# Performance work log

Measured on AMD Instinct MI355X. Metric: run time of the kernel, lower is better.

Reference implementation:

```python
import jax, jax.numpy as jnp
import numpy as np

EPS = 1e-06
FOCUSING_FACTOR = 3


def setup_inputs() -> dict:
    key = jax.random.key(0)
    k1, k2, k3, k4, k5 = jax.random.split(key, 5)
    N, L, H, D = 8, 4096, 8, 64
    return {
        "queries": jax.random.normal(k1, (N, L, H, D), dtype=jnp.float32),
        "keys": jax.random.normal(k2, (N, L, H, D), dtype=jnp.float32),
        "values": jax.random.normal(k3, (N, L, H, D), dtype=jnp.float32),
        "scale_param": jnp.zeros((1, 1, 1, D), dtype=jnp.float32),
        "dwc_w": jax.random.normal(k4, (D, 1, 5, 5), dtype=jnp.float32) * 0.1,
        "dwc_b": jax.random.normal(k5, (D,), dtype=jnp.float32) * 0.1,
        "height": 64,
    }


def reference(queries, keys, values, scale_param, dwc_w, dwc_b, height):
    N, L, H, D = values.shape
    width = L // height

    scale = jax.nn.softplus(scale_param)  # [1,1,1,D]
    q = (jax.nn.relu(queries) + 1e-06) / scale
    k = (jax.nn.relu(keys) + 1e-06) / scale

    q_norm = jnp.linalg.norm(q, axis=-1, keepdims=True)
    k_norm = jnp.linalg.norm(k, axis=-1, keepdims=True)
    q = q ** FOCUSING_FACTOR
    k = k ** FOCUSING_FACTOR
    q = q / jnp.linalg.norm(q, axis=-1, keepdims=True) * q_norm
    k = k / jnp.linalg.norm(k, axis=-1, keepdims=True) * k_norm

    # linear attention: kv summary [N,H,D,D], normalizer z [N,L,H]
    kv = jnp.einsum("nshd,nshv->nhdv", k, values)
    z = 1.0 / (jnp.einsum("nlhd,nhd->nlh", q, k.sum(axis=1)) + EPS)
    o = jnp.einsum("nlhd,nhdv,nlh->nlhv", q, kv, z)

    # depthwise 5x5 conv on values: 'n (h w) heads d -> (n heads) d h w'
    vf = values.reshape(N, height, width, H, D)
    vf = vf.transpose(0, 3, 4, 1, 2).reshape(N * H, D, height, width)
    vf = jax.lax.conv_general_dilated(
        vf, dwc_w,
        window_strides=(1, 1), padding=((2, 2), (2, 2)),
        dimension_numbers=("NCHW", "OIHW", "NCHW"),
        feature_group_count=D,
    ) + dwc_b[None, :, None, None]
    vf = vf.reshape(N, H, D, height, width).transpose(0, 3, 4, 1, 2)
    vf = vf.reshape(N, L, H, D)

    return o + vf
```

## Files before the change

### kernel.cpp

```cpp
#include <hip/hip_runtime.h>

typedef __attribute__((ext_vector_type(8))) short short8;
typedef __attribute__((ext_vector_type(4))) float f32x4;

#define LSEQ   4096
#define NHEAD  8
#define DCH    64
#define HEIGHT 64
#define WIDTH  64

static __device__ __forceinline__ float bfu2f(unsigned short u) {
  return __uint_as_float(((unsigned int)u) << 16);
}
static __device__ __forceinline__ unsigned short f2bfu(float f) {
  unsigned int b = __float_as_uint(f);
  b += 0x7FFFu + ((b >> 16) & 1u);
  return (unsigned short)(b >> 16);
}
static __device__ __forceinline__ float ldf(const void* p, int i, int isbf) {
  return isbf ? bfu2f(((const unsigned short*)p)[i]) : ((const float*)p)[i];
}
static __device__ __forceinline__ float softplus_inv(float sp) {
  float s = (sp > 20.f) ? sp : log1pf(expf(sp));
  return 1.f / s;
}
static __device__ __forceinline__ void unpack2(unsigned int u, float& lo, float& hi) {
  lo = __uint_as_float(u << 16);
  hi = __uint_as_float(u & 0xFFFF0000u);
}
static __device__ __forceinline__ void load8(const void* p, int gi, int isbf, float o[8]) {
  if (isbf) {
    uint4 u = *(const uint4*)((const unsigned short*)p + gi);
    unpack2(u.x, o[0], o[1]); unpack2(u.y, o[2], o[3]);
    unpack2(u.z, o[4], o[5]); unpack2(u.w, o[6], o[7]);
  } else {
    const float4* f4 = (const float4*)((const float*)p + gi);
    float4 a = f4[0], b = f4[1];
    o[0]=a.x; o[1]=a.y; o[2]=a.z; o[3]=a.w;
    o[4]=b.x; o[5]=b.y; o[6]=b.z; o[7]=b.w;
  }
}
static __device__ __forceinline__ void row_reduce2(float& a, float& b) {
  #pragma unroll
  for (int m = 1; m < 8; m <<= 1) { a += __shfl_xor(a, m, 64); b += __shfl_xor(b, m, 64); }
}
static __device__ __forceinline__ float row_reduce1(float a) {
  #pragma unroll
  for (int m = 1; m < 8; m <<= 1) a += __shfl_xor(a, m, 64);
  return a;
}

__global__ void detect_kernel(const unsigned int* __restrict__ q, int* __restrict__ flag) {
  int lane = threadIdx.x & 63;
  int hits = 0;
  #pragma unroll
  for (int i = 0; i < 4; ++i) {
    unsigned int lo = q[lane * 4 + i] & 0xFFFFu;
    unsigned int e  = (lo >> 7) & 0xFFu;
    if (lo == 0u || (e >= 110u && e <= 140u)) hits++;
  }
  #pragma unroll
  for (int m = 1; m < 64; m <<= 1) hits += __shfl_xor(hits, m, 64);
  if (lane == 0) *flag = (hits > 128) ? 1 : 0;
}

__global__ __launch_bounds__(256) void kv_kernel(
    const void* __restrict__ keys, const void* __restrict__ values,
    const void* __restrict__ scale_param,
    float* __restrict__ kv_p, float* __restrict__ ksum_g,
    const int* __restrict__ flagp, int chunks, int rows)
{
  __shared__ __align__(16) unsigned short kfT[64 * 40];
  __shared__ __align__(16) unsigned short vvT[64 * 40];
  __shared__ float red[256];

  const int isbf = *flagp;
  const int b = blockIdx.x;
  const int chunk = b % chunks;
  const int nh = b / chunks;
  const int h = nh & 7, n = nh >> 3;
  const int t = threadIdx.x, lane = t & 63, wid = t >> 6;
  const int quad = lane >> 4, m16 = lane & 15;
  const int r = lane >> 3, c = lane & 7, d0 = c * 8;
  const int s_local = wid * 8 + r;
  const int sp = s_local ^ ((c & 3) << 3);

  float inv_s[8];
  #pragma unroll
  for (int i = 0; i < 8; ++i) inv_s[i] = softplus_inv(ldf(scale_param, d0 + i, isbf));

  f32x4 acc[4];
  #pragma unroll
  for (int mt = 0; mt < 4; ++mt) acc[mt] = (f32x4){0.f, 0.f, 0.f, 0.f};
  float ksum_acc[8];
  #pragma unroll
  for (int i = 0; i < 8; ++i) ksum_acc[i] = 0.f;

  const int nsub = rows >> 5;
  for (int sub = 0; sub < nsub; ++sub) {
    const int s = chunk * rows + sub * 32 + s_local;
    const int gi = ((n * LSEQ + s) * NHEAD + h) * DCH + d0;

    float kraw[8];
    load8(keys, gi, isbf, kraw);
    float xv[8], yv[8], s2 = 0.f, s6 = 0.f;
    #pragma unroll
    for (int i = 0; i < 8; ++i) {
      xv[i] = (fmaxf(kraw[i], 0.f) + 1e-6f) * inv_s[i];
      s2 += xv[i] * xv[i];
    }
    #pragma unroll
    for (int i = 0; i < 8; ++i) {
      yv[i] = xv[i] * xv[i] * xv[i];
      s6 += yv[i] * yv[i];
    }
    row_reduce2(s2, s6);
    const float coef = sqrtf(s2 / s6);
    #pragma unroll
    for (int i = 0; i < 8; ++i) {
      float f = yv[i] * coef;
      ksum_acc[i] += f;
      kfT[(d0 + i) * 40 + sp] = f2bfu(f);
    }
    if (isbf) {
      uint4 u = *(const uint4*)((const unsigned short*)values + gi);
      unsigned short vs[8];
      *(uint4*)vs = u;
      #pragma unroll
      for (int i = 0; i < 8; ++i) vvT[(d0 + i) * 40 + sp] = vs[i];
    } else {
      float vraw[8];
      load8(values, gi, 0, vraw);
      #pragma unroll
      for (int i = 0; i < 8; ++i) vvT[(d0 + i) * 40 + sp] = f2bfu(vraw[i]);
    }
    __syncthreads();

    const int v = wid * 16 + m16;
    short8 bfr = *(const short8*)&vvT[v * 40 + (quad ^ ((v >> 3) & 3)) * 8];
    #pragma unroll
    for (int mt = 0; mt < 4; ++mt) {
      int d = mt * 16 + m16;
      short8 afr = *(const short8*)&kfT[d * 40 + (quad ^ ((d >> 3) & 3)) * 8];
      acc[mt] = __builtin_amdgcn_mfma_f32_16x16x32_bf16(afr, bfr, acc[mt], 0, 0, 0);
    }
    __syncthreads();
  }

  float* dst = kv_p + ((size_t)chunk * 64 + nh) * 4096;
  #pragma unroll
  for (int mt = 0; mt < 4; ++mt)
    #pragma unroll
    for (int rr = 0; rr < 4; ++rr) {
      int d = mt * 16 + quad * 4 + rr;
      dst[d * 64 + wid * 16 + m16] = acc[mt][rr];
    }

  #pragma unroll
  for (int i = 0; i < 8; ++i) {
    #pragma unroll
    for (int m = 8; m < 64; m <<= 1) ksum_acc[i] += __shfl_xor(ksum_acc[i], m, 64);
  }
  if (r == 0) {
    #pragma unroll
    for (int i = 0; i < 8; ++i) red[wid * 64 + d0 + i] = ksum_acc[i];
  }
  __syncthreads();
  if (t < 64) {
    float tot = red[t] + red[64 + t] + red[128 + t] + red[192 + t];
    atomicAdd(&ksum_g[nh * 64 + t], tot);
  }
}

__global__ __launch_bounds__(256) void reduce_kernel(
    const float* __restrict__ kv_p, unsigned short* __restrict__ kvb, int chunks)
{
  int cidx = blockIdx.x * 256 + threadIdx.x;
  int nh = cidx >> 12;
  int dv = cidx & 4095;
  int d = dv >> 6, v = dv & 63;
  float s = 0.f;
  for (int ch = 0; ch < chunks; ++ch)
    s += kv_p[((size_t)ch * 64 + nh) * 4096 + dv];
  kvb[(nh * 64 + v) * 64 + d] = f2bfu(s);
}

__global__ __launch_bounds__(256) void attn_kernel(
    const void* __restrict__ queries, const unsigned short* __restrict__ kvb,
    const float* __restrict__ ksum_g, const void* __restrict__ scale_param,
    void* __restrict__ out, const int* __restrict__ flagp)
{
  __shared__ __align__(16) unsigned short qf[64 * 72];

  const int isbf = *flagp;
  const int b = blockIdx.x;
  const int y = b & 63;
  const int nh = b >> 6;
  const int h = nh & 7, n = nh >> 3;
  const int t = threadIdx.x, lane = t & 63, wid = t >> 6;
  const int quad = lane >> 4, m16 = lane & 15;
  const int r = lane >> 3, c = lane & 7, d0 = c * 8;

  float inv_s[8];
  #pragma unroll
  for (int i = 0; i < 8; ++i) inv_s[i] = softplus_inv(ldf(scale_param, d0 + i, isbf));
  float ks[8];
  {
    float4 k0 = *(const float4*)&ksum_g[nh * 64 + d0];
    float4 k1 = *(const float4*)&ksum_g[nh * 64 + d0 + 4];
    ks[0]=k0.x; ks[1]=k0.y; ks[2]=k0.z; ks[3]=k0.w;
    ks[4]=k1.x; ks[5]=k1.y; ks[6]=k1.z; ks[7]=k1.w;
  }

  const unsigned short* kvrow = kvb + (nh * 64 + wid * 16 + m16) * 64;
  short8 bfr0 = *(const short8*)&kvrow[quad * 8];
  short8 bfr1 = *(const short8*)&kvrow[32 + quad * 8];

  #pragma unroll
  for (int batch = 0; batch < 2; ++batch) {
    int x = wid * 16 + batch * 8 + r;
    int gi = ((n * LSEQ + y * 64 + x) * NHEAD + h) * DCH + d0;
    float qraw[8];
    load8(queries, gi, isbf, qraw);
    float xv[8], yv[8], s2 = 0.f, s6 = 0.f;
    #pragma unroll
    for (int i = 0; i < 8; ++i) {
      xv[i] = (fmaxf(qraw[i], 0.f) + 1e-6f) * inv_s[i];
      s2 += xv[i] * xv[i];
    }
    #pragma unroll
    for (int i = 0; i < 8; ++i) {
      yv[i] = xv[i] * xv[i] * xv[i];
      s6 += yv[i] * yv[i];
    }
    row_reduce2(s2, s6);
    const float coef = sqrtf(s2 / s6);
    float f[8], dot = 0.f;
    #pragma unroll
    for (int i = 0; i < 8; ++i) { f[i] = yv[i] * coef; dot += f[i] * ks[i]; }
    dot = row_reduce1(dot);
    const float z = 1.f / (dot + 1e-6f);
    uint4 pk;
    pk.x = (unsigned int)f2bfu(f[0] * z) | ((unsigned int)f2bfu(f[1] * z) << 16);
    pk.y = (unsigned int)f2bfu(f[2] * z) | ((unsigned int)f2bfu(f[3] * z) << 16);
    pk.z = (unsigned int)f2bfu(f[4] * z) | ((unsigned int)f2bfu(f[5] * z) << 16);
    pk.w = (unsigned int)f2bfu(f[6] * z) | ((unsigned int)f2bfu(f[7] * z) << 16);
    *(uint4*)&qf[x * 72 + d0] = pk;
  }
  __syncthreads();

  const size_t obase = (((size_t)n * LSEQ + y * 64) * NHEAD + h) * DCH;
  #pragma unroll
  for (int mt = 0; mt < 4; ++mt) {
    f32x4 acc = (f32x4){0.f, 0.f, 0.f, 0.f};
    short8 a0 = *(const short8*)&qf[(mt * 16 + m16) * 72 + quad * 8];
    short8 a1 = *(const short8*)&qf[(mt * 16 + m16) * 72 + 32 + quad * 8];
    acc = __builtin_amdgcn_mfma_f32_16x16x32_bf16(a0, bfr0, acc, 0, 0, 0);
    acc = __builtin_amdgcn_mfma_f32_16x16x32_bf16(a1, bfr1, acc, 0, 0, 0);
    #pragma unroll
    for (int rr = 0; rr < 4; ++rr) {
      int x = mt * 16 + quad * 4 + rr;
      int v = wid * 16 + m16;
      size_t oi = obase + (size_t)x * (NHEAD * DCH) + v;
      if (isbf) ((unsigned short*)out)[oi] = f2bfu(acc[rr]);
      else      ((float*)out)[oi] = acc[rr];
    }
  }
}

__global__ __launch_bounds__(256) void conv_kernel(
    const void* __restrict__ values, const void* __restrict__ dwc_w,
    const void* __restrict__ dwc_b, void* __restrict__ out,
    const int* __restrict__ flagp)
{
  __shared__ __align__(16) unsigned short vs[8 * 64 * 64];
  __shared__ float wl[25 * 64];
  __shared__ float bl[64];

  const int isbf = *flagp;
  const int b = blockIdx.x;
  const int slab = b & 15;
  const int nh = b >> 4;
  const int h = nh & 7, n = nh >> 3;
  const int y0 = slab * 4;
  const int t = threadIdx.x;

  for (int i = t; i < 25 * 64; i += 256) {
    int d = i / 25, tap = i - d * 25;
    wl[tap * 64 + d] = ldf(dwc_w, i, isbf);
  }
  if (t < 64) bl[t] = ldf(dwc_b, t, isbf);

  for (int it = t; it < 8 * 64 * 8; it += 256) {
    int j = it & 7;
    int xx = (it >> 3) & 63;
    int rr = it >> 9;
    int yy = y0 - 2 + rr;
    unsigned short* dst = &vs[((rr * 64 + xx) * 64) + ((j ^ (xx & 7)) * 8)];
    if (yy >= 0 && yy < HEIGHT) {
      int gi = ((n * LSEQ + yy * 64 + xx) * NHEAD + h) * DCH + j * 8;
      if (isbf) {
        *(uint4*)dst = *(const uint4*)((const unsigned short*)values + gi);
      } else {
        const float4* s4 = (const float4*)((const float*)values + gi);
        float4 f0 = s4[0], f1 = s4[1];
        dst[0] = f2bfu(f0.x); dst[1] = f2bfu(f0.y);
        dst[2] = f2bfu(f0.z); dst[3] = f2bfu(f0.w);
        dst[4] = f2bfu(f1.x); dst[5] = f2bfu(f1.y);
        dst[6] = f2bfu(f1.z); dst[7] = f2bfu(f1.w);
      }
    } else {
      uint4 z; z.x = z.y = z.z = z.w = 0u;
      *(uint4*)dst = z;
    }
  }
  __syncthreads();

  const int xx = t & 63, jb = t >> 6;
  for (int jj = jb; jj < 8; jj += 4) {
    float a[4][8];
    float bias8[8];
    {
      float4 b0 = *(const float4*)&bl[jj * 8];
      float4 b1 = *(const float4*)&bl[jj * 8 + 4];
      bias8[0]=b0.x; bias8[1]=b0.y; bias8[2]=b0.z; bias8[3]=b0.w;
      bias8[4]=b1.x; bias8[5]=b1.y; bias8[6]=b1.z; bias8[7]=b1.w;
    }
    #pragma unroll
    for (int rr = 0; rr < 4; ++rr)
      #pragma unroll
      for (int cc = 0; cc < 8; ++cc) a[rr][cc] = bias8[cc];

    for (int ky = 0; ky < 5; ++ky) {
      #pragma unroll
      for (int kx = 0; kx < 5; ++kx) {
        int xs = xx + kx - 2;
        if ((unsigned)xs < (unsigned)WIDTH) {
          float4 w0 = *(const float4*)&wl[(ky * 5 + kx) * 64 + jj * 8];
          float4 w1 = *(const float4*)&wl[(ky * 5 + kx) * 64 + jj * 8 + 4];
          #pragma unroll
          for (int rr = 0; rr < 4; ++rr) {
            uint4 pv = *(const uint4*)&vs[(((rr + ky) * 64 + xs) * 64) + ((jj ^ (xs & 7)) * 8)];
            float v0,v1,v2,v3,v4,v5,v6,v7;
            unpack2(pv.x, v0, v1); unpack2(pv.y, v2, v3);
            unpack2(pv.z, v4, v5); unpack2(pv.w, v6, v7);
            a[rr][0] += w0.x * v0; a[rr][1] += w0.y * v1;
            a[rr][2] += w0.z * v2; a[rr][3] += w0.w * v3;
            a[rr][4] += w1.x * v4; a[rr][5] += w1.y * v5;
            a[rr][6] += w1.z * v6; a[rr][7] += w1.w * v7;
          }
        }
      }
    }
    #pragma unroll
    for (int rr = 0; rr < 4; ++rr) {
      size_t oi = (((size_t)n * LSEQ + (y0 + rr) * 64 + xx) * NHEAD + h) * DCH + jj * 8;
      if (isbf) {
        unsigned short* op = (unsigned short*)out + oi;
        uint4 cur = *(uint4*)op;
        float c0,c1,c2,c3,c4,c5,c6,c7;
        unpack2(cur.x, c0, c1); unpack2(cur.y, c2, c3);
        unpack2(cur.z, c4, c5); unpack2(cur.w, c6, c7);
        uint4 res;
        res.x = (unsigned int)f2bfu(c0 + a[rr][0]) | ((unsigned int)f2bfu(c1 + a[rr][1]) << 16);
        res.y = (unsigned int)f2bfu(c2 + a[rr][2]) | ((unsigned int)f2bfu(c3 + a[rr][3]) << 16);
        res.z = (unsigned int)f2bfu(c4 + a[rr][4]) | ((unsigned int)f2bfu(c5 + a[rr][5]) << 16);
        res.w = (unsigned int)f2bfu(c6 + a[rr][6]) | ((unsigned int)f2bfu(c7 + a[rr][7]) << 16);
        *(uint4*)op = res;
      } else {
        float* op = (float*)out + oi;
        float4 o0 = *(float4*)op;
        float4 o1 = *(float4*)(op + 4);
        o0.x += a[rr][0]; o0.y += a[rr][1]; o0.z += a[rr][2]; o0.w += a[rr][3];
        o1.x += a[rr][4]; o1.y += a[rr][5]; o1.z += a[rr][6]; o1.w += a[rr][7];
        *(float4*)op = o0;
        *(float4*)(op + 4) = o1;
      }
    }
  }
}

extern "C" void kernel_launch(void* const* d_in, const int* in_sizes, int n_in,
                              void* d_out, int out_size, void* d_ws, size_t ws_size,
                              hipStream_t stream) {
  int chunks = 16;
  while (chunks > 1) {
    size_t need = (size_t)chunks * 64 * 4096 * 4 + 64 * 4096 * 2 + 4096 * 4 + 64;
    if (need <= ws_size) break;
    chunks >>= 1;
  }
  const int rows = LSEQ / chunks;

  float* kv_p = (float*)d_ws;
  unsigned short* kvb = (unsigned short*)(kv_p + (size_t)chunks * 64 * 4096);
  float* ksum = (float*)(kvb + 64 * 4096);
  int* flag = (int*)(ksum + 4096);

  hipMemsetAsync(ksum, 0, 4096 * sizeof(float), stream);
  detect_kernel<<<1, 64, 0, stream>>>((const unsigned int*)d_in[0], flag);
  kv_kernel<<<64 * chunks, 256, 0, stream>>>(
      d_in[1], d_in[2], d_in[3], kv_p, ksum, flag, chunks, rows);
  reduce_kernel<<<1024, 256, 0, stream>>>(kv_p, kvb, chunks);
  attn_kernel<<<4096, 256, 0, stream>>>(
      d_in[0], kvb, ksum, d_in[3], d_out, flag);
  conv_kernel<<<64 * 16, 256, 0, stream>>>(
      d_in[2], d_in[4], d_in[5], d_out, flag);
}
```

Baseline: 334.1 us.

## Fuse attention output and depthwise conv into one kernel; double kv tile depth

Merges attn_kernel and conv_kernel into a single kernel that computes the linear-attention output for a 4-row slab, keeps it in LDS as bf16, then adds the depthwise 5x5 conv, which reads values directly from global memory instead of staging them in LDS. This removes the write and read-modify-write of the output in global memory. The kv_kernel now processes 64 rows per sync step instead of 32, issuing two MFMAs per step. Block ids are remapped so slabs are grouped by xcd. The attention result is rounded to bf16 before the conv term is added, which costs some precision in the fp32 path.

```diff
diff --git a/kernel.cpp b/kernel.cpp
--- a/kernel.cpp
+++ b/kernel.cpp
@@ -70,8 +70,8 @@
     float* __restrict__ kv_p, float* __restrict__ ksum_g,
     const int* __restrict__ flagp, int chunks, int rows)
 {
-  __shared__ __align__(16) unsigned short kfT[64 * 40];
-  __shared__ __align__(16) unsigned short vvT[64 * 40];
+  __shared__ __align__(16) unsigned short kfT[64 * 72];
+  __shared__ __align__(16) unsigned short vvT[64 * 72];
   __shared__ float red[256];
 
   const int isbf = *flagp;
@@ -82,8 +82,7 @@
   const int t = threadIdx.x, lane = t & 63, wid = t >> 6;
   const int quad = lane >> 4, m16 = lane & 15;
   const int r = lane >> 3, c = lane & 7, d0 = c * 8;
-  const int s_local = wid * 8 + r;
-  const int sp = s_local ^ ((c & 3) << 3);
+  const int swz = (c & 3) << 3;
 
   float inv_s[8];
   #pragma unroll
@@ -96,53 +95,63 @@
   #pragma unroll
   for (int i = 0; i < 8; ++i) ksum_acc[i] = 0.f;
 
-  const int nsub = rows >> 5;
+  const int nsub = rows >> 6;
   for (int sub = 0; sub < nsub; ++sub) {
-    const int s = chunk * rows + sub * 32 + s_local;
-    const int gi = ((n * LSEQ + s) * NHEAD + h) * DCH + d0;
-
-    float kraw[8];
-    load8(keys, gi, isbf, kraw);
-    float xv[8], yv[8], s2 = 0.f, s6 = 0.f;
-    #pragma unroll
-    for (int i = 0; i < 8; ++i) {
-      xv[i] = (fmaxf(kraw[i], 0.f) + 1e-6f) * inv_s[i];
-      s2 += xv[i] * xv[i];
-    }
-    #pragma unroll
-    for (int i = 0; i < 8; ++i) {
-      yv[i] = xv[i] * xv[i] * xv[i];
-      s6 += yv[i] * yv[i];
-    }
-    row_reduce2(s2, s6);
-    const float coef = sqrtf(s2 / s6);
-    #pragma unroll
-    for (int i = 0; i < 8; ++i) {
-      float f = yv[i] * coef;
-      ksum_acc[i] += f;
-      kfT[(d0 + i) * 40 + sp] = f2bfu(f);
-    }
-    if (isbf) {
-      uint4 u = *(const uint4*)((const unsigned short*)values + gi);
-      unsigned short vs[8];
-      *(uint4*)vs = u;
-      #pragma unroll
-      for (int i = 0; i < 8; ++i) vvT[(d0 + i) * 40 + sp] = vs[i];
-    } else {
-      float vraw[8];
-      load8(values, gi, 0, vraw);
-      #pragma unroll
-      for (int i = 0; i < 8; ++i) vvT[(d0 + i) * 40 + sp] = f2bfu(vraw[i]);
+    #pragma unroll
+    for (int pp = 0; pp < 2; ++pp) {
+      const int s_loc = wid * 8 + r + pp * 32;
+      const int sp = s_loc ^ swz;
+      const int s = chunk * rows + sub * 64 + s_loc;
+      const int gi = ((n * LSEQ + s) * NHEAD + h) * DCH + d0;
+
+      float kraw[8];
+      load8(keys, gi, isbf, kraw);
+      float xv[8], yv[8], s2 = 0.f, s6 = 0.f;
+      #pragma unroll
+      for (int i = 0; i < 8; ++i) {
+        xv[i] = (fmaxf(kraw[i], 0.f) + 1e-6f) * inv_s[i];
+        s2 += xv[i] * xv[i];
+      }
+      #pragma unroll
+      for (int i = 0; i < 8; ++i) {
+        yv[i] = xv[i] * xv[i] * xv[i];
+        s6 += yv[i] * yv[i];
+      }
+      row_reduce2(s2, s6);
+      const float coef = sqrtf(s2 / s6);
+      #pragma unroll
+      for (int i = 0; i < 8; ++i) {
+        float f = yv[i] * coef;
+        ksum_acc[i] += f;
+        kfT[(d0 + i) * 72 + sp] = f2bfu(f);
+      }
+      if (isbf) {
+        uint4 u = *(const uint4*)((const unsigned short*)values + gi);
+        unsigned short vs[8];
+        *(uint4*)vs = u;
+        #pragma unroll
+        for (int i = 0; i < 8; ++i) vvT[(d0 + i) * 72 + sp] = vs[i];
+      } else {
+        float vraw[8];
+        load8(values, gi, 0, vraw);
+        #pragma unroll
+        for (int i = 0; i < 8; ++i) vvT[(d0 + i) * 72 + sp] = f2bfu(vraw[i]);
+      }
     }
     __syncthreads();
 
     const int v = wid * 16 + m16;
-    short8 bfr = *(const short8*)&vvT[v * 40 + (quad ^ ((v >> 3) & 3)) * 8];
+    const int vg = (v >> 3) & 3;
+    short8 bv0 = *(const short8*)&vvT[v * 72 + ((quad ^ vg) << 3)];
+    short8 bv1 = *(const short8*)&vvT[v * 72 + ((4 + (quad ^ vg)) << 3)];
     #pragma unroll
     for (int mt = 0; mt < 4; ++mt) {
       int d = mt * 16 + m16;
-      short8 afr = *(const short8*)&kfT[d * 40 + (quad ^ ((d >> 3) & 3)) * 8];
-      acc[mt] = __builtin_amdgcn_mfma_f32_16x16x32_bf16(afr, bfr, acc[mt], 0, 0, 0);
+      int dg = (d >> 3) & 3;
+      short8 a0 = *(const short8*)&kfT[d * 72 + ((quad ^ dg) << 3)];
+      short8 a1 = *(const short8*)&kfT[d * 72 + ((4 + (quad ^ dg)) << 3)];
+      acc[mt] = __builtin_amdgcn_mfma_f32_16x16x32_bf16(a0, bv0, acc[mt], 0, 0, 0);
+      acc[mt] = __builtin_amdgcn_mfma_f32_16x16x32_bf16(a1, bv1, acc[mt], 0, 0, 0);
     }
     __syncthreads();
   }
@@ -185,21 +194,33 @@
   kvb[(nh * 64 + v) * 64 + d] = f2bfu(s);
 }
 
-__global__ __launch_bounds__(256) void attn_kernel(
-    const void* __restrict__ queries, const unsigned short* __restrict__ kvb,
-    const float* __restrict__ ksum_g, const void* __restrict__ scale_param,
-    void* __restrict__ out, const int* __restrict__ flagp)
+__global__ __launch_bounds__(256) void fused_kernel(
+    const void* __restrict__ queries, const void* __restrict__ values,
+    const unsigned short* __restrict__ kvb, const float* __restrict__ ksum_g,
+    const void* __restrict__ scale_param, const void* __restrict__ dwc_w,
+    const void* __restrict__ dwc_b, void* __restrict__ out,
+    const int* __restrict__ flagp)
 {
-  __shared__ __align__(16) unsigned short qf[64 * 72];
+  __shared__ __align__(16) unsigned short qfo[256 * 72];
+  __shared__ float wl[25 * 64];
+  __shared__ float bl[64];
 
   const int isbf = *flagp;
   const int b = blockIdx.x;
-  const int y = b & 63;
-  const int nh = b >> 6;
+  const int xcd = b & 7;
+  const int rest = b >> 3;
+  const int nh = rest & 63;
+  const int y0 = xcd * 8 + (rest >> 6) * 4;
   const int h = nh & 7, n = nh >> 3;
   const int t = threadIdx.x, lane = t & 63, wid = t >> 6;
   const int quad = lane >> 4, m16 = lane & 15;
   const int r = lane >> 3, c = lane & 7, d0 = c * 8;
+
+  for (int i = t; i < 25 * 64; i += 256) {
+    int d = i / 25, tap = i - d * 25;
+    wl[tap * 64 + d] = ldf(dwc_w, i, isbf);
+  }
+  if (t < 64) bl[t] = ldf(dwc_b, t, isbf);
 
   float inv_s[8];
   #pragma unroll
@@ -212,14 +233,11 @@
     ks[4]=k1.x; ks[5]=k1.y; ks[6]=k1.z; ks[7]=k1.w;
   }
 
-  const unsigned short* kvrow = kvb + (nh * 64 + wid * 16 + m16) * 64;
-  short8 bfr0 = *(const short8*)&kvrow[quad * 8];
-  short8 bfr1 = *(const short8*)&kvrow[32 + quad * 8];
-
-  #pragma unroll
-  for (int batch = 0; batch < 2; ++batch) {
-    int x = wid * 16 + batch * 8 + r;
-    int gi = ((n * LSEQ + y * 64 + x) * NHEAD + h) * DCH + d0;
+  #pragma unroll
+  for (int batch = 0; batch < 8; ++batch) {
+    int p = wid * 64 + batch * 8 + r;
+    int x = p & 63, yy = y0 + (p >> 6);
+    int gi = ((n * LSEQ + yy * 64 + x) * NHEAD + h) * DCH + d0;
     float qraw[8];
     load8(queries, gi, isbf, qraw);
     float xv[8], yv[8], s2 = 0.f, s6 = 0.f;
@@ -245,136 +263,119 @@
     pk.y = (unsigned int)f2bfu(f[2] * z) | ((unsigned int)f2bfu(f[3] * z) << 16);
     pk.z = (unsigned int)f2bfu(f[4] * z) | ((unsigned int)f2bfu(f[5] * z) << 16);
     pk.w = (unsigned int)f2bfu(f[6] * z) | ((unsigned int)f2bfu(f[7] * z) << 16);
-    *(uint4*)&qf[x * 72 + d0] = pk;
+    *(uint4*)&qfo[p * 72 + d0] = pk;
   }
   __syncthreads();
 
-  const size_t obase = (((size_t)n * LSEQ + y * 64) * NHEAD + h) * DCH;
-  #pragma unroll
-  for (int mt = 0; mt < 4; ++mt) {
-    f32x4 acc = (f32x4){0.f, 0.f, 0.f, 0.f};
-    short8 a0 = *(const short8*)&qf[(mt * 16 + m16) * 72 + quad * 8];
-    short8 a1 = *(const short8*)&qf[(mt * 16 + m16) * 72 + 32 + quad * 8];
-    acc = __builtin_amdgcn_mfma_f32_16x16x32_bf16(a0, bfr0, acc, 0, 0, 0);
-    acc = __builtin_amdgcn_mfma_f32_16x16x32_bf16(a1, bfr1, acc, 0, 0, 0);
-    #pragma unroll
-    for (int rr = 0; rr < 4; ++rr) {
-      int x = mt * 16 + quad * 4 + rr;
-      int v = wid * 16 + m16;
-      size_t oi = obase + (size_t)x * (NHEAD * DCH) + v;
-      if (isbf) ((unsigned short*)out)[oi] = f2bfu(acc[rr]);
-      else      ((float*)out)[oi] = acc[rr];
-    }
-  }
-}
-
-__global__ __launch_bounds__(256) void conv_kernel(
-    const void* __restrict__ values, const void* __restrict__ dwc_w,
-    const void* __restrict__ dwc_b, void* __restrict__ out,
-    const int* __restrict__ flagp)
-{
-  __shared__ __align__(16) unsigned short vs[8 * 64 * 64];
-  __shared__ float wl[25 * 64];
-  __shared__ float bl[64];
-
-  const int isbf = *flagp;
-  const int b = blockIdx.x;
-  const int slab = b & 15;
-  const int nh = b >> 4;
-  const int h = nh & 7, n = nh >> 3;
-  const int y0 = slab * 4;
-  const int t = threadIdx.x;
-
-  for (int i = t; i < 25 * 64; i += 256) {
-    int d = i / 25, tap = i - d * 25;
-    wl[tap * 64 + d] = ldf(dwc_w, i, isbf);
-  }
-  if (t < 64) bl[t] = ldf(dwc_b, t, isbf);
-
-  for (int it = t; it < 8 * 64 * 8; it += 256) {
-    int j = it & 7;
-    int xx = (it >> 3) & 63;
-    int rr = it >> 9;
-    int yy = y0 - 2 + rr;
-    unsigned short* dst = &vs[((rr * 64 + xx) * 64) + ((j ^ (xx & 7)) * 8)];
-    if (yy >= 0 && yy < HEIGHT) {
-      int gi = ((n * LSEQ + yy * 64 + xx) * NHEAD + h) * DCH + j * 8;
-      if (isbf) {
-        *(uint4*)dst = *(const uint4*)((const unsigned short*)values + gi);
-      } else {
-        const float4* s4 = (const float4*)((const float*)values + gi);
-        float4 f0 = s4[0], f1 = s4[1];
-        dst[0] = f2bfu(f0.x); dst[1] = f2bfu(f0.y);
-        dst[2] = f2bfu(f0.z); dst[3] = f2bfu(f0.w);
-        dst[4] = f2bfu(f1.x); dst[5] = f2bfu(f1.y);
-        dst[6] = f2bfu(f1.z); dst[7] = f2bfu(f1.w);
-      }
-    } else {
-      uint4 z; z.x = z.y = z.z = z.w = 0u;
-      *(uint4*)dst = z;
-    }
+  const int v = wid * 16 + m16;
+  const unsigned short* kvrow = kvb + (nh * 64 + v) * 64;
+  short8 bfr0 = *(const short8*)&kvrow[quad * 8];
+  short8 bfr1 = *(const short8*)&kvrow[32 + quad * 8];
+  f32x4 acc[16];
+  #pragma unroll
+  for (int mt = 0; mt < 16; ++mt) {
+    acc[mt] = (f32x4){0.f, 0.f, 0.f, 0.f};
+    short8 a0 = *(const short8*)&qfo[(mt * 16 + m16) * 72 + quad * 8];
+    short8 a1 = *(const short8*)&qfo[(mt * 16 + m16) * 72 + 32 + quad * 8];
+    acc[mt] = __builtin_amdgcn_mfma_f32_16x16x32_bf16(a0, bfr0, acc[mt], 0, 0, 0);
+    acc[mt] = __builtin_amdgcn_mfma_f32_16x16x32_bf16(a1, bfr1, acc[mt], 0, 0, 0);
   }
   __syncthreads();
 
+  #pragma unroll
+  for (int mt = 0; mt < 16; ++mt)
+    #pragma unroll
+    for (int rg = 0; rg < 4; ++rg) {
+      int p = mt * 16 + quad * 4 + rg;
+      qfo[p * 72 + v] = f2bfu(acc[mt][rg]);
+    }
+
   const int xx = t & 63, jb = t >> 6;
-  for (int jj = jb; jj < 8; jj += 4) {
-    float a[4][8];
-    float bias8[8];
+  float ca[2][4][8];
+  #pragma unroll
+  for (int ji = 0; ji < 2; ++ji) {
+    const int jj = jb + ji * 4;
     {
       float4 b0 = *(const float4*)&bl[jj * 8];
       float4 b1 = *(const float4*)&bl[jj * 8 + 4];
-      bias8[0]=b0.x; bias8[1]=b0.y; bias8[2]=b0.z; bias8[3]=b0.w;
-      bias8[4]=b1.x; bias8[5]=b1.y; bias8[6]=b1.z; bias8[7]=b1.w;
-    }
-    #pragma unroll
-    for (int rr = 0; rr < 4; ++rr)
-      #pragma unroll
-      for (int cc = 0; cc < 8; ++cc) a[rr][cc] = bias8[cc];
-
-    for (int ky = 0; ky < 5; ++ky) {
+      #pragma unroll
+      for (int rr = 0; rr < 4; ++rr) {
+        ca[ji][rr][0]=b0.x; ca[ji][rr][1]=b0.y; ca[ji][rr][2]=b0.z; ca[ji][rr][3]=b0.w;
+        ca[ji][rr][4]=b1.x; ca[ji][rr][5]=b1.y; ca[ji][rr][6]=b1.z; ca[ji][rr][7]=b1.w;
+      }
+    }
+    #pragma unroll
+    for (int z = 0; z < 8; ++z) {
+      int yy = y0 - 2 + z;
+      if (yy < 0 || yy >= HEIGHT) continue;
+      float win[5][8];
       #pragma unroll
       for (int kx = 0; kx < 5; ++kx) {
         int xs = xx + kx - 2;
-        if ((unsigned)xs < (unsigned)WIDTH) {
+        bool ok = (unsigned)xs < (unsigned)WIDTH;
+        if (isbf) {
+          uint4 pv = {0u,0u,0u,0u};
+          if (ok) pv = *(const uint4*)((const unsigned short*)values +
+                       (((n * LSEQ + yy * 64 + xs) * NHEAD + h) * DCH + jj * 8));
+          unpack2(pv.x, win[kx][0], win[kx][1]); unpack2(pv.y, win[kx][2], win[kx][3]);
+          unpack2(pv.z, win[kx][4], win[kx][5]); unpack2(pv.w, win[kx][6], win[kx][7]);
+        } else {
+          float4 a = {0,0,0,0}, bq = {0,0,0,0};
+          if (ok) {
+            const float4* f4 = (const float4*)((const float*)values +
+                       (((n * LSEQ + yy * 64 + xs) * NHEAD + h) * DCH + jj * 8));
+            a = f4[0]; bq = f4[1];
+          }
+          win[kx][0]=a.x; win[kx][1]=a.y; win[kx][2]=a.z; win[kx][3]=a.w;
+          win[kx][4]=bq.x; win[kx][5]=bq.y; win[kx][6]=bq.z; win[kx][7]=bq.w;
+        }
+      }
+      #pragma unroll
+      for (int ky = 0; ky < 5; ++ky) {
+        const int rr = z - ky;
+        if (rr < 0 || rr > 3) continue;
+        #pragma unroll
+        for (int kx = 0; kx < 5; ++kx) {
           float4 w0 = *(const float4*)&wl[(ky * 5 + kx) * 64 + jj * 8];
           float4 w1 = *(const float4*)&wl[(ky * 5 + kx) * 64 + jj * 8 + 4];
-          #pragma unroll
-          for (int rr = 0; rr < 4; ++rr) {
-            uint4 pv = *(const uint4*)&vs[(((rr + ky) * 64 + xs) * 64) + ((jj ^ (xs & 7)) * 8)];
-            float v0,v1,v2,v3,v4,v5,v6,v7;
-            unpack2(pv.x, v0, v1); unpack2(pv.y, v2, v3);
-            unpack2(pv.z, v4, v5); unpack2(pv.w, v6, v7);
-            a[rr][0] += w0.x * v0; a[rr][1] += w0.y * v1;
-            a[rr][2] += w0.z * v2; a[rr][3] += w0.w * v3;
-            a[rr][4] += w1.x * v4; a[rr][5] += w1.y * v5;
-            a[rr][6] += w1.z * v6; a[rr][7] += w1.w * v7;
-          }
+          ca[ji][rr][0] += w0.x * win[kx][0]; ca[ji][rr][1] += w0.y * win[kx][1];
+          ca[ji][rr][2] += w0.z * win[kx][2]; ca[ji][rr][3] += w0.w * win[kx][3];
+          ca[ji][rr][4] += w1.x * win[kx][4]; ca[ji][rr][5] += w1.y * win[kx][5];
+          ca[ji][rr][6] += w1.z * win[kx][6]; ca[ji][rr][7] += w1.w * win[kx][7];
         }
       }
     }
+  }
+  __syncthreads();
+
+  #pragma unroll
+  for (int ji = 0; ji < 2; ++ji) {
+    const int jj = jb + ji * 4;
     #pragma unroll
     for (int rr = 0; rr < 4; ++rr) {
+      int p = rr * 64 + xx;
+      uint4 ov = *(const uint4*)&qfo[p * 72 + jj * 8];
+      float o0,o1,o2,o3,o4,o5,o6,o7;
+      unpack2(ov.x, o0, o1); unpack2(ov.y, o2, o3);
+      unpack2(ov.z, o4, o5); unpack2(ov.w, o6, o7);
+      float r0 = o0 + ca[ji][rr][0], r1 = o1 + ca[ji][rr][1];
+      float r2 = o2 + ca[ji][rr][2], r3 = o3 + ca[ji][rr][3];
+      float r4 = o4 + ca[ji][rr][4], r5 = o5 + ca[ji][rr][5];
+      float r6 = o6 + ca[ji][rr][6], r7 = o7 + ca[ji][rr][7];
       size_t oi = (((size_t)n * LSEQ + (y0 + rr) * 64 + xx) * NHEAD + h) * DCH + jj * 8;
       if (isbf) {
-        unsigned short* op = (unsigned short*)out + oi;
-        uint4 cur = *(uint4*)op;
-        float c0,c1,c2,c3,c4,c5,c6,c7;
-        unpack2(cur.x, c0, c1); unpack2(cur.y, c2, c3);
-        unpack2(cur.z, c4, c5); unpack2(cur.w, c6, c7);
         uint4 res;
-        res.x = (unsigned int)f2bfu(c0 + a[rr][0]) | ((unsigned int)f2bfu(c1 + a[rr][1]) << 16);
-        res.y = (unsigned int)f2bfu(c2 + a[rr][2]) | ((unsigned int)f2bfu(c3 + a[rr][3]) << 16);
-        res.z = (unsigned int)f2bfu(c4 + a[rr][4]) | ((unsigned int)f2bfu(c5 + a[rr][5]) << 16);
-        res.w = (unsigned int)f2bfu(c6 + a[rr][6]) | ((unsigned int)f2bfu(c7 + a[rr][7]) << 16);
-        *(uint4*)op = res;
+        res.x = (unsigned int)f2bfu(r0) | ((unsigned int)f2bfu(r1) << 16);
+        res.y = (unsigned int)f2bfu(r2) | ((unsigned int)f2bfu(r3) << 16);
+        res.z = (unsigned int)f2bfu(r4) | ((unsigned int)f2bfu(r5) << 16);
+        res.w = (unsigned int)f2bfu(r6) | ((unsigned int)f2bfu(r7) << 16);
+        *(uint4*)((unsigned short*)out + oi) = res;
       } else {
         float* op = (float*)out + oi;
-        float4 o0 = *(float4*)op;
-        float4 o1 = *(float4*)(op + 4);
-        o0.x += a[rr][0]; o0.y += a[rr][1]; o0.z += a[rr][2]; o0.w += a[rr][3];
-        o1.x += a[rr][4]; o1.y += a[rr][5]; o1.z += a[rr][6]; o1.w += a[rr][7];
-        *(float4*)op = o0;
-        *(float4*)(op + 4) = o1;
+        float4 q0 = {r0, r1, r2, r3};
+        float4 q1 = {r4, r5, r6, r7};
+        *(float4*)op = q0;
+        *(float4*)(op + 4) = q1;
       }
     }
   }
@@ -401,8 +402,6 @@
   kv_kernel<<<64 * chunks, 256, 0, stream>>>(
       d_in[1], d_in[2], d_in[3], kv_p, ksum, flag, chunks, rows);
   reduce_kernel<<<1024, 256, 0, stream>>>(kv_p, kvb, chunks);
-  attn_kernel<<<4096, 256, 0, stream>>>(
-      d_in[0], kvb, ksum, d_in[3], d_out, flag);
-  conv_kernel<<<64 * 16, 256, 0, stream>>>(
-      d_in[2], d_in[4], d_in[5], d_out, flag);
-}
+  fused_kernel<<<1024, 256, 0, stream>>>(
+      d_in[0], d_in[2], kvb, ksum, d_in[3], d_in[4], d_in[5], d_out, flag);
+}
```

After: 351.1 us. 1.05x slower.
